# Kernel optimization log

Measured on AMD Instinct MI355X. Metric: run time of the kernel, lower is better.

## Reference

```python
import jax, jax.numpy as jnp
import numpy as np

D = 1024  # in_features == latent_dim
EPS = 1e-5


def _layernorm(x, g, b):
    mu = jnp.mean(x, axis=-1, keepdims=True)
    var = jnp.mean(jnp.square(x - mu), axis=-1, keepdims=True)
    return (x - mu) * jax.lax.rsqrt(var + EPS) * g + b


def setup_inputs() -> dict:
    key = jax.random.key(0)
    ks = jax.random.split(key, 8)
    s = 1.0 / np.sqrt(D)
    return {
        "x": jax.random.normal(ks[0], (4, 4096, D), dtype=jnp.float32),
        "w_qkv": jax.random.uniform(ks[1], (3 * D, D), jnp.float32, -s, s),
        "w_o": jax.random.uniform(ks[2], (D, D), jnp.float32, -s, s),
        "w1": jax.random.uniform(ks[3], (D, D), jnp.float32, -s, s),
        "b1": jax.random.uniform(ks[4], (D,), jnp.float32, -s, s),
        "w2": jax.random.uniform(ks[5], (D, D), jnp.float32, -s, s),
        "b2": jax.random.uniform(ks[6], (D,), jnp.float32, -s, s),
        "ln1_g": jnp.ones((D,), jnp.float32),
        "ln1_b": jnp.zeros((D,), jnp.float32),
        "ln2_g": jnp.ones((D,), jnp.float32),
        "ln2_b": jnp.zeros((D,), jnp.float32),
    }


def reference(x, w_qkv, w_o, w1, b1, w2, b2, ln1_g, ln1_b, ln2_g, ln2_b):
    B, S, _ = x.shape
    scale = 1.0 / np.sqrt(D * 1)  # 1/sqrt(latent_dim * n_heads), n_heads=1
    qkv = jnp.einsum("bsd,ed->bse", x, w_qkv)            # [B,S,3D]
    qkv = qkv.reshape(B, S, 1, 3 * D).transpose(0, 2, 1, 3)  # [B,1,S,3D]
    q, k, v = jnp.split(qkv, 3, axis=-1)                  # each [B,1,S,D]
    logits = jnp.einsum("bhid,bhjd->bhij", q, k) * scale  # [B,1,S,S]
    # Faithful quirk: softmax over the HEAD axis (dim=1). With 1 head this
    # yields an all-ones attention matrix.
    attn = jax.nn.softmax(logits, axis=1)
    vals = jnp.einsum("bhij,bhjd->bhid", attn, v)         # [B,1,S,D]
    vals = vals.transpose(0, 2, 1, 3).reshape(B, S, D)
    attn_out = jnp.einsum("bsd,ed->bse", vals, w_o)
    # squeeze(-2) is a no-op for S>1
    x = _layernorm(x + attn_out, ln1_g, ln1_b)
    h = jax.nn.gelu(jnp.einsum("bsd,ed->bse", x, w1) + b1, approximate=False)
    mlp_out = jnp.einsum("bsd,ed->bse", h, w2) + b2
    return _layernorm(x + mlp_out, ln2_g, ln2_b)
```

## Files before the change

kernel.cpp:

```cpp
#include <hip/hip_runtime.h>
#include <hip/hip_bf16.h>

typedef __hip_bfloat16 bf16;
typedef __attribute__((ext_vector_type(8))) short short8;
typedef __attribute__((ext_vector_type(4))) float f32x4;

#define DDIM 1024
#define SEQ  4096
#define NB   4
#define MTOT (NB*SEQ)

static __device__ __forceinline__ unsigned short f2bf(float f) {
    __hip_bfloat16 h = __float2bfloat16(f);
    unsigned short u; __builtin_memcpy(&u, &h, 2); return u;
}
static __device__ __forceinline__ float bf2f(unsigned short u) {
    __hip_bfloat16 h; __builtin_memcpy(&h, &u, 2); return __bfloat162float(h);
}

__global__ __launch_bounds__(256) void cast_w_kernel(
    const float* __restrict__ w1, const float* __restrict__ w2,
    unsigned short* __restrict__ w1b, unsigned short* __restrict__ w2b)
{
    size_t idx = ((size_t)blockIdx.x*256 + threadIdx.x) * 4;
    float4 a = *(const float4*)(w1 + idx);
    ushort4 o; o.x=f2bf(a.x); o.y=f2bf(a.y); o.z=f2bf(a.z); o.w=f2bf(a.w);
    *(ushort4*)(w1b + idx) = o;
    float4 b = *(const float4*)(w2 + idx);
    o.x=f2bf(b.x); o.y=f2bf(b.y); o.z=f2bf(b.z); o.w=f2bf(b.w);
    *(ushort4*)(w2b + idx) = o;
}

__global__ __launch_bounds__(256) void colsum_partial_kernel(
    const float* __restrict__ x, float* __restrict__ partial)
{
    int d  = blockIdx.x*256 + threadIdx.x;
    int b  = blockIdx.y;
    int sl = blockIdx.z;
    const float* p = x + ((size_t)b*SEQ + (size_t)sl*128)*DDIM + d;
    float s = 0.f;
    #pragma unroll 4
    for (int i = 0; i < 128; ++i) s += p[(size_t)i*DDIM];
    partial[((size_t)sl*NB + b)*DDIM + d] = s;
}

__global__ __launch_bounds__(256) void colsum_reduce_kernel(
    const float* __restrict__ partial, float* __restrict__ xsum)
{
    int d = blockIdx.x*256 + threadIdx.x;
    int b = blockIdx.y;
    float s = 0.f;
    #pragma unroll
    for (int sl = 0; sl < 32; ++sl) s += partial[((size_t)sl*NB + b)*DDIM + d];
    xsum[b*DDIM + d] = s;
}

__global__ __launch_bounds__(256) void matvec_kernel(
    const float* __restrict__ W, const float* __restrict__ vin, float* __restrict__ vout)
{
    int b = blockIdx.y;
    int g = threadIdx.x >> 4;
    int t = threadIdx.x & 15;
    int e = blockIdx.x*16 + g;
    const float* w = W + (size_t)e*DDIM;
    const float* v = vin + b*DDIM;
    float s = 0.f;
    for (int k = t; k < DDIM; k += 16) s += w[k]*v[k];
    #pragma unroll
    for (int o = 8; o; o >>= 1) s += __shfl_down(s, o, 16);
    if (t == 0) vout[b*DDIM + e] = s;
}

__global__ __launch_bounds__(256) void ln1_kernel(
    const float* __restrict__ x, const float* __restrict__ avec,
    const float* __restrict__ g1, const float* __restrict__ b1,
    unsigned short* __restrict__ x1b)
{
    int row = blockIdx.x;
    int b   = row >> 12;
    int tid = threadIdx.x;
    const float4* xr = (const float4*)(x + (size_t)row*DDIM);
    const float4* av = (const float4*)(avec + (size_t)b*DDIM);
    float4 xv = xr[tid], a4 = av[tid];
    float y0 = xv.x+a4.x, y1 = xv.y+a4.y, y2 = xv.z+a4.z, y3 = xv.w+a4.w;
    float s  = y0+y1+y2+y3;
    float ss = y0*y0+y1*y1+y2*y2+y3*y3;
    #pragma unroll
    for (int o = 32; o; o >>= 1) { s += __shfl_down(s,o,64); ss += __shfl_down(ss,o,64); }
    __shared__ float red[8];
    if ((tid&63) == 0) { red[tid>>6] = s; red[4+(tid>>6)] = ss; }
    __syncthreads();
    float St = red[0]+red[1]+red[2]+red[3];
    float Sq = red[4]+red[5]+red[6]+red[7];
    float mu = St*(1.0f/DDIM);
    float rs = rsqrtf(Sq*(1.0f/DDIM) - mu*mu + 1e-5f);
    float4 g4 = ((const float4*)g1)[tid];
    float4 bb = ((const float4*)b1)[tid];
    ushort4 o;
    o.x = f2bf((y0-mu)*rs*g4.x + bb.x);
    o.y = f2bf((y1-mu)*rs*g4.y + bb.y);
    o.z = f2bf((y2-mu)*rs*g4.z + bb.z);
    o.w = f2bf((y3-mu)*rs*g4.w + bb.w);
    *(ushort4*)(x1b + (size_t)row*DDIM + tid*4) = o;
}

__global__ __launch_bounds__(256, 3) void gemm_s32_kernel(
    const bf16* __restrict__ A, const bf16* __restrict__ Bw,
    const float* __restrict__ bias, unsigned short* __restrict__ outb)
{
    constexpr int K = 1024, N = 1024, BK = 32;
    __shared__ __align__(16) bf16 As[128*BK];
    __shared__ __align__(16) bf16 Bs[128*BK];
    const int tid  = threadIdx.x;
    const int wave = tid >> 6, lane = tid & 63;

    int bid = blockIdx.x;
    int swz = (bid & 7) * 128 + (bid >> 3);
    const size_t bm = (size_t)(swz >> 3) * 128;
    const size_t bn = (size_t)(swz & 7) * 128;

    const int wr = (wave >> 1) * 64, wc = (wave & 1) * 64;
    const int fr = lane & 15, fs = lane >> 4;

    const int srow = lane >> 2;
    const int sk   = (((lane & 3) ^ ((lane >> 3) & 3)) << 3);

    const int swo = (fs ^ ((fr >> 1) & 3)) << 4;

    f32x4 acc[4][4] = {};
    const bf16* Ab = A  + bm * K;
    const bf16* Bb = Bw + bn * K;

    for (int kt = 0; kt < K; kt += BK) {
        #pragma unroll
        for (int c = 0; c < 2; ++c) {
            int chunk = c*4 + wave;
            const bf16* ga = Ab + (size_t)(chunk*16 + srow)*K + kt + sk;
            const bf16* gb = Bb + (size_t)(chunk*16 + srow)*K + kt + sk;
            __builtin_amdgcn_global_load_lds(
                (const __attribute__((address_space(1))) void*)ga,
                (__attribute__((address_space(3))) void*)((char*)As + chunk*1024), 16, 0, 0);
            __builtin_amdgcn_global_load_lds(
                (const __attribute__((address_space(1))) void*)gb,
                (__attribute__((address_space(3))) void*)((char*)Bs + chunk*1024), 16, 0, 0);
        }
        __syncthreads();
        short8 af[4], bfr[4];
        #pragma unroll
        for (int m = 0; m < 4; ++m) af[m]  = *(const short8*)((char*)As + (wr + m*16 + fr)*64 + swo);
        #pragma unroll
        for (int n = 0; n < 4; ++n) bfr[n] = *(const short8*)((char*)Bs + (wc + n*16 + fr)*64 + swo);
        __builtin_amdgcn_s_setprio(1);
        #pragma unroll
        for (int m = 0; m < 4; ++m)
            #pragma unroll
            for (int n = 0; n < 4; ++n)
                acc[m][n] = __builtin_amdgcn_mfma_f32_16x16x32_bf16(af[m], bfr[n], acc[m][n], 0, 0, 0);
        __builtin_amdgcn_s_setprio(0);
        __syncthreads();
    }

    const int crow = fs * 4, ccol = fr;
    #pragma unroll
    for (int n = 0; n < 4; ++n) {
        size_t col = bn + wc + n*16 + ccol;
        float bv = bias[col];
        #pragma unroll
        for (int m = 0; m < 4; ++m) {
            #pragma unroll
            for (int r = 0; r < 4; ++r) {
                size_t row = bm + wr + m*16 + crow + r;
                float v = acc[m][n][r] + bv;
                float ge = 0.5f*v*(1.0f + erff(v*0.70710678118f));
                outb[row*(size_t)N + col] = f2bf(ge);
            }
        }
    }
}

__global__ __launch_bounds__(256, 2) void gemm2_kernel(
    const bf16* __restrict__ A, const bf16* __restrict__ Bw,
    const float* __restrict__ bias, unsigned short* __restrict__ xy,
    float2* __restrict__ part)
{
    constexpr int K = 1024, N = 1024, BK = 64, NT = K / BK;
    __shared__ __align__(16) bf16 lds[2][2][128*BK];
    const int tid  = threadIdx.x;
    const int wave = tid >> 6, lane = tid & 63;

    int bid = blockIdx.x;
    int swz = (bid & 7) * 128 + (bid >> 3);
    const size_t bm = (size_t)(swz >> 3) * 128;
    const size_t bn = (size_t)(swz & 7) * 128;

    const int wm = wave >> 1;
    const int wn = wave & 1;

    const int srow = tid >> 3;
    const int skel = (((tid & 7) ^ ((tid >> 3) & 7)) << 3);

    const int fr = lane & 15;
    const int fs = lane >> 4;
    int foff[2];
    #pragma unroll
    for (int ks = 0; ks < 2; ++ks)
        foff[ks] = fr*128 + (((ks*4 + fs) ^ (fr & 7)) << 4);

    f32x4 acc[4][4] = {};
    const bf16* Ab = A  + bm * K;
    const bf16* Bb = Bw + bn * K;

    auto stage = [&](int b, int kt) {
        #pragma unroll
        for (int mat = 0; mat < 2; ++mat) {
            const bf16* src = (mat == 0 ? Ab : Bb);
            #pragma unroll
            for (int g = 0; g < 4; ++g) {
                int row = g*32 + srow;
                const bf16* gp = src + (size_t)row * K + kt*BK + skel;
                __builtin_amdgcn_global_load_lds(
                    (const __attribute__((address_space(1))) void*)gp,
                    (__attribute__((address_space(3))) void*)
                        ((char*)&lds[b][mat][0] + g*4096 + wave*1024),
                    16, 0, 0);
            }
        }
    };

    stage(0, 0);

    #pragma unroll 2
    for (int t = 0; t < NT; ++t) {
        const int cur = t & 1;
        if (t < NT-1) {
            stage(cur ^ 1, t + 1);
            asm volatile("s_waitcnt vmcnt(8)" ::: "memory");
        } else {
            asm volatile("s_waitcnt vmcnt(0)" ::: "memory");
        }
        __builtin_amdgcn_s_barrier();

        const char* LA = (const char*)&lds[cur][0][0] + wm*8192;
        const char* LB = (const char*)&lds[cur][1][0] + wn*8192;
        #pragma unroll
        for (int ks = 0; ks < 2; ++ks) {
            short8 af[4], bfr[4];
            #pragma unroll
            for (int m = 0; m < 4; ++m) af[m]  = *(const short8*)(LA + m*2048 + foff[ks]);
            #pragma unroll
            for (int n = 0; n < 4; ++n) bfr[n] = *(const short8*)(LB + n*2048 + foff[ks]);
            __builtin_amdgcn_s_setprio(1);
            #pragma unroll
            for (int m = 0; m < 4; ++m)
                #pragma unroll
                for (int n = 0; n < 4; ++n)
                    acc[m][n] = __builtin_amdgcn_mfma_f32_16x16x32_bf16(
                        af[m], bfr[n], acc[m][n], 0, 0, 0);
            __builtin_amdgcn_s_setprio(0);
        }
        __builtin_amdgcn_s_barrier();
    }

    float vs[4][4] = {}, vq[4][4] = {};
    #pragma unroll
    for (int n = 0; n < 4; ++n) {
        size_t col = bn + wn*64 + n*16 + fr;
        float bv = bias[col];
        #pragma unroll
        for (int m = 0; m < 4; ++m) {
            #pragma unroll
            for (int r = 0; r < 4; ++r) {
                size_t row = bm + wm*64 + m*16 + fs*4 + r;
                size_t idx = row*(size_t)N + col;
                float v = acc[m][n][r] + bv + bf2f(xy[idx]);
                unsigned short qb = f2bf(v);
                xy[idx] = qb;
                float vv = bf2f(qb);
                vs[m][r] += vv;
                vq[m][r] += vv*vv;
            }
        }
    }
    #pragma unroll
    for (int o = 1; o < 16; o <<= 1) {
        #pragma unroll
        for (int m = 0; m < 4; ++m)
            #pragma unroll
            for (int r = 0; r < 4; ++r) {
                vs[m][r] += __shfl_xor(vs[m][r], o);
                vq[m][r] += __shfl_xor(vq[m][r], o);
            }
    }
    float* lred = (float*)&lds[0][0][0];
    if (fr == 0) {
        #pragma unroll
        for (int m = 0; m < 4; ++m)
            #pragma unroll
            for (int r = 0; r < 4; ++r) {
                int rl = wm*64 + m*16 + fs*4 + r;
                lred[(wn*128 + rl)*2]     = vs[m][r];
                lred[(wn*128 + rl)*2 + 1] = vq[m][r];
            }
    }
    __syncthreads();
    if (tid < 128) {
        float s  = lred[tid*2]       + lred[(128 + tid)*2];
        float sq = lred[tid*2 + 1]   + lred[(128 + tid)*2 + 1];
        part[(bm + tid)*8 + (bn >> 7)] = make_float2(s, sq);
    }
}

__global__ __launch_bounds__(256) void ln2_apply_kernel(
    const unsigned short* __restrict__ yb, const float2* __restrict__ part,
    const float* __restrict__ g2, const float* __restrict__ b2,
    float* __restrict__ out)
{
    int row = blockIdx.x;
    int tid = threadIdx.x;
    float s = 0.f, sq = 0.f;
    #pragma unroll
    for (int i = 0; i < 8; ++i) {
        float2 p = part[(size_t)row*8 + i];
        s += p.x; sq += p.y;
    }
    float mu = s * (1.0f/DDIM);
    float rs = rsqrtf(sq * (1.0f/DDIM) - mu*mu + 1e-5f);
    ushort4 yv = *(const ushort4*)(yb + (size_t)row*DDIM + tid*4);
    float4 g4 = ((const float4*)g2)[tid];
    float4 bb = ((const float4*)b2)[tid];
    float4 o;
    o.x = (bf2f(yv.x) - mu)*rs*g4.x + bb.x;
    o.y = (bf2f(yv.y) - mu)*rs*g4.y + bb.y;
    o.z = (bf2f(yv.z) - mu)*rs*g4.z + bb.z;
    o.w = (bf2f(yv.w) - mu)*rs*g4.w + bb.w;
    ((float4*)(out + (size_t)row*DDIM))[tid] = o;
}

extern "C" void kernel_launch(void* const* d_in, const int* in_sizes, int n_in,
                              void* d_out, int out_size, void* d_ws, size_t ws_size,
                              hipStream_t stream)
{
    const float* x     = (const float*)d_in[0];
    const float* w_qkv = (const float*)d_in[1];
    const float* w_o   = (const float*)d_in[2];
    const float* w1    = (const float*)d_in[3];
    const float* b1    = (const float*)d_in[4];
    const float* w2    = (const float*)d_in[5];
    const float* b2    = (const float*)d_in[6];
    const float* ln1g  = (const float*)d_in[7];
    const float* ln1b  = (const float*)d_in[8];
    const float* ln2g  = (const float*)d_in[9];
    const float* ln2b  = (const float*)d_in[10];
    float* out = (float*)d_out;
    char* ws = (char*)d_ws;

    unsigned short* x1b = (unsigned short*)(ws);
    unsigned short* hb  = (unsigned short*)(ws + 33554432);
    unsigned short* w1b = (unsigned short*)(ws + 67108864);
    unsigned short* w2b = (unsigned short*)(ws + 69206016);
    float* partial = (float*)(ws + 71303168);
    float* xsum    = (float*)(ws + 71827456);
    float* tvec    = (float*)(ws + 71843840);
    float* avec    = (float*)(ws + 71860224);
    float2* lnpart = (float2*)(ws + 67108864);

    cast_w_kernel<<<dim3(1024), 256, 0, stream>>>(w1, w2, w1b, w2b);
    colsum_partial_kernel<<<dim3(4, NB, 32), 256, 0, stream>>>(x, partial);
    colsum_reduce_kernel<<<dim3(4, NB), 256, 0, stream>>>(partial, xsum);
    matvec_kernel<<<dim3(64, NB), 256, 0, stream>>>(w_qkv + (size_t)2*DDIM*DDIM, xsum, tvec);
    matvec_kernel<<<dim3(64, NB), 256, 0, stream>>>(w_o, tvec, avec);
    ln1_kernel<<<dim3(MTOT), 256, 0, stream>>>(x, avec, ln1g, ln1b, x1b);
    gemm_s32_kernel<<<dim3(1024), 256, 0, stream>>>(
        (const bf16*)x1b, (const bf16*)w1b, b1, hb);
    gemm2_kernel<<<dim3(1024), 256, 0, stream>>>(
        (const bf16*)hb, (const bf16*)w2b, b2, x1b, lnpart);
    ln2_apply_kernel<<<dim3(MTOT), 256, 0, stream>>>(x1b, lnpart, ln2g, ln2b, out);
}
```

Baseline: 174.8 us.

## Double-buffer LDS tiles in first MLP GEMM with async prefetch

The first MLP GEMM now keeps two LDS buffers and issues the global-to-LDS loads for the next K tile before computing on the current one. It waits on vmcnt so only the previous tile's loads must finish, and uses raw s_barrier in place of __syncthreads. Launch bounds rise from 3 to 4 blocks per CU. The aim is to hide global load latency behind the MFMA work, at the cost of twice the LDS per block, which may limit occupancy.

```diff
diff --git a/kernel.cpp b/kernel.cpp
--- a/kernel.cpp
+++ b/kernel.cpp
@@ -104,13 +104,12 @@
     *(ushort4*)(x1b + (size_t)row*DDIM + tid*4) = o;
 }
 
-__global__ __launch_bounds__(256, 3) void gemm_s32_kernel(
+__global__ __launch_bounds__(256, 4) void gemm_bk32_kernel(
     const bf16* __restrict__ A, const bf16* __restrict__ Bw,
     const float* __restrict__ bias, unsigned short* __restrict__ outb)
 {
-    constexpr int K = 1024, N = 1024, BK = 32;
-    __shared__ __align__(16) bf16 As[128*BK];
-    __shared__ __align__(16) bf16 Bs[128*BK];
+    constexpr int K = 1024, N = 1024, BK = 32, NT = K / BK;
+    __shared__ __align__(16) bf16 lds[2][2][128*BK];
     const int tid  = threadIdx.x;
     const int wave = tid >> 6, lane = tid & 63;
 
@@ -122,8 +121,8 @@
     const int wr = (wave >> 1) * 64, wc = (wave & 1) * 64;
     const int fr = lane & 15, fs = lane >> 4;
 
-    const int srow = lane >> 2;
-    const int sk   = (((lane & 3) ^ ((lane >> 3) & 3)) << 3);
+    const int srow = tid >> 2;
+    const int sk   = (((tid & 3) ^ ((tid >> 3) & 3)) << 3);
 
     const int swo = (fs ^ ((fr >> 1) & 3)) << 4;
 
@@ -131,25 +130,42 @@
     const bf16* Ab = A  + bm * K;
     const bf16* Bb = Bw + bn * K;
 
-    for (int kt = 0; kt < K; kt += BK) {
-        #pragma unroll
-        for (int c = 0; c < 2; ++c) {
-            int chunk = c*4 + wave;
-            const bf16* ga = Ab + (size_t)(chunk*16 + srow)*K + kt + sk;
-            const bf16* gb = Bb + (size_t)(chunk*16 + srow)*K + kt + sk;
-            __builtin_amdgcn_global_load_lds(
-                (const __attribute__((address_space(1))) void*)ga,
-                (__attribute__((address_space(3))) void*)((char*)As + chunk*1024), 16, 0, 0);
-            __builtin_amdgcn_global_load_lds(
-                (const __attribute__((address_space(1))) void*)gb,
-                (__attribute__((address_space(3))) void*)((char*)Bs + chunk*1024), 16, 0, 0);
-        }
-        __syncthreads();
+    auto stage = [&](int b, int kt) {
+        #pragma unroll
+        for (int mat = 0; mat < 2; ++mat) {
+            const bf16* src = (mat == 0 ? Ab : Bb);
+            #pragma unroll
+            for (int g = 0; g < 2; ++g) {
+                const bf16* gp = src + (size_t)(g*64 + srow) * K + kt*BK + sk;
+                __builtin_amdgcn_global_load_lds(
+                    (const __attribute__((address_space(1))) void*)gp,
+                    (__attribute__((address_space(3))) void*)
+                        ((char*)&lds[b][mat][0] + g*4096 + wave*1024),
+                    16, 0, 0);
+            }
+        }
+    };
+
+    stage(0, 0);
+
+    #pragma unroll 2
+    for (int t = 0; t < NT; ++t) {
+        const int cur = t & 1;
+        if (t < NT-1) {
+            stage(cur ^ 1, t + 1);
+            asm volatile("s_waitcnt vmcnt(4)" ::: "memory");
+        } else {
+            asm volatile("s_waitcnt vmcnt(0)" ::: "memory");
+        }
+        __builtin_amdgcn_s_barrier();
+
+        const char* LA = (const char*)&lds[cur][0][0];
+        const char* LB = (const char*)&lds[cur][1][0];
         short8 af[4], bfr[4];
         #pragma unroll
-        for (int m = 0; m < 4; ++m) af[m]  = *(const short8*)((char*)As + (wr + m*16 + fr)*64 + swo);
-        #pragma unroll
-        for (int n = 0; n < 4; ++n) bfr[n] = *(const short8*)((char*)Bs + (wc + n*16 + fr)*64 + swo);
+        for (int m = 0; m < 4; ++m) af[m]  = *(const short8*)(LA + (wr + m*16 + fr)*64 + swo);
+        #pragma unroll
+        for (int n = 0; n < 4; ++n) bfr[n] = *(const short8*)(LB + (wc + n*16 + fr)*64 + swo);
         __builtin_amdgcn_s_setprio(1);
         #pragma unroll
         for (int m = 0; m < 4; ++m)
@@ -157,13 +173,13 @@
             for (int n = 0; n < 4; ++n)
                 acc[m][n] = __builtin_amdgcn_mfma_f32_16x16x32_bf16(af[m], bfr[n], acc[m][n], 0, 0, 0);
         __builtin_amdgcn_s_setprio(0);
-        __syncthreads();
-    }
-
-    const int crow = fs * 4, ccol = fr;
+        __builtin_amdgcn_s_barrier();
+    }
+
+    const int crow = fs * 4;
     #pragma unroll
     for (int n = 0; n < 4; ++n) {
-        size_t col = bn + wc + n*16 + ccol;
+        size_t col = bn + wc + n*16 + fr;
         float bv = bias[col];
         #pragma unroll
         for (int m = 0; m < 4; ++m) {
@@ -370,7 +386,7 @@
     matvec_kernel<<<dim3(64, NB), 256, 0, stream>>>(w_qkv + (size_t)2*DDIM*DDIM, xsum, tvec);
     matvec_kernel<<<dim3(64, NB), 256, 0, stream>>>(w_o, tvec, avec);
     ln1_kernel<<<dim3(MTOT), 256, 0, stream>>>(x, avec, ln1g, ln1b, x1b);
-    gemm_s32_kernel<<<dim3(1024), 256, 0, stream>>>(
+    gemm_bk32_kernel<<<dim3(1024), 256, 0, stream>>>(
         (const bf16*)x1b, (const bf16*)w1b, b1, hb);
     gemm2_kernel<<<dim3(1024), 256, 0, stream>>>(
         (const bf16*)hb, (const bf16*)w2b, b2, x1b, lnpart);
```

After: 173.0 us. Within noise of the previous version (-1.0%).

## Replace first MLP GEMM with 256x256-tile 8-wave double-buffered pipelined kernel

Applied to the files above, without the earlier changes.

Swaps the 128x128, BK=32, single-buffered GEMM1 (x1·w1ᵀ + bias + GELU) for a 256x256 tile kernel with 8 waves and 128 KB of dynamic LDS. Loads are double-buffered at BK=64 and interleaved with MFMA phases using explicit vmcnt/lgkmcnt waits and barriers. The aim is more data reuse per tile and overlap of global→LDS transfers with compute. In exchange it launches only 256 blocks at one block per CU, relies on fragile hand-placed waitcnts, and the larger accumulator file raises register pressure.

```diff
diff --git a/kernel.cpp b/kernel.cpp
--- a/kernel.cpp
+++ b/kernel.cpp
@@ -104,78 +104,120 @@
     *(ushort4*)(x1b + (size_t)row*DDIM + tid*4) = o;
 }
 
-__global__ __launch_bounds__(256, 3) void gemm_s32_kernel(
+__global__ __launch_bounds__(512, 1) void gemm8p_kernel(
     const bf16* __restrict__ A, const bf16* __restrict__ Bw,
     const float* __restrict__ bias, unsigned short* __restrict__ outb)
 {
-    constexpr int K = 1024, N = 1024, BK = 32;
-    __shared__ __align__(16) bf16 As[128*BK];
-    __shared__ __align__(16) bf16 Bs[128*BK];
+    extern __shared__ char smem[];
     const int tid  = threadIdx.x;
     const int wave = tid >> 6, lane = tid & 63;
 
     int bid = blockIdx.x;
-    int swz = (bid & 7) * 128 + (bid >> 3);
-    const size_t bm = (size_t)(swz >> 3) * 128;
-    const size_t bn = (size_t)(swz & 7) * 128;
-
-    const int wr = (wave >> 1) * 64, wc = (wave & 1) * 64;
+    int swz = (bid & 7) * 32 + (bid >> 3);
+    const size_t bm = (size_t)(swz >> 2) * 256;
+    const size_t bn = (size_t)(swz & 3) * 256;
+
+    const int wm = wave >> 2;
+    const int wn = wave & 3;
+
+    const int srow = tid >> 3;
+    const int skel = (((tid & 7) ^ ((tid >> 3) & 7)) << 3);
     const int fr = lane & 15, fs = lane >> 4;
 
-    const int srow = lane >> 2;
-    const int sk   = (((lane & 3) ^ ((lane >> 3) & 3)) << 3);
-
-    const int swo = (fs ^ ((fr >> 1) & 3)) << 4;
-
-    f32x4 acc[4][4] = {};
-    const bf16* Ab = A  + bm * K;
-    const bf16* Bb = Bw + bn * K;
-
-    for (int kt = 0; kt < K; kt += BK) {
-        #pragma unroll
-        for (int c = 0; c < 2; ++c) {
-            int chunk = c*4 + wave;
-            const bf16* ga = Ab + (size_t)(chunk*16 + srow)*K + kt + sk;
-            const bf16* gb = Bb + (size_t)(chunk*16 + srow)*K + kt + sk;
-            __builtin_amdgcn_global_load_lds(
-                (const __attribute__((address_space(1))) void*)ga,
-                (__attribute__((address_space(3))) void*)((char*)As + chunk*1024), 16, 0, 0);
-            __builtin_amdgcn_global_load_lds(
-                (const __attribute__((address_space(1))) void*)gb,
-                (__attribute__((address_space(3))) void*)((char*)Bs + chunk*1024), 16, 0, 0);
-        }
-        __syncthreads();
-        short8 af[4], bfr[4];
-        #pragma unroll
-        for (int m = 0; m < 4; ++m) af[m]  = *(const short8*)((char*)As + (wr + m*16 + fr)*64 + swo);
-        #pragma unroll
-        for (int n = 0; n < 4; ++n) bfr[n] = *(const short8*)((char*)Bs + (wc + n*16 + fr)*64 + swo);
-        __builtin_amdgcn_s_setprio(1);
-        #pragma unroll
-        for (int m = 0; m < 4; ++m)
-            #pragma unroll
-            for (int n = 0; n < 4; ++n)
-                acc[m][n] = __builtin_amdgcn_mfma_f32_16x16x32_bf16(af[m], bfr[n], acc[m][n], 0, 0, 0);
-        __builtin_amdgcn_s_setprio(0);
-        __syncthreads();
-    }
-
-    const int crow = fs * 4, ccol = fr;
-    #pragma unroll
-    for (int n = 0; n < 4; ++n) {
-        size_t col = bn + wc + n*16 + ccol;
+    const bf16* Ab = A  + bm * 1024;
+    const bf16* Bb = Bw + bn * 1024;
+
+#define REGN(d,mat,h) (smem + ((((d)<<2)|((mat)<<1)|(h))<<14))
+#define STAGE(dst, srcb, kt) { \
+    _Pragma("unroll") for (int g_ = 0; g_ < 2; ++g_) { \
+        const bf16* gp_ = (srcb) + (size_t)(g_*64 + srow)*1024 + (kt)*64 + skel; \
+        __builtin_amdgcn_global_load_lds( \
+            (const __attribute__((address_space(1))) void*)gp_, \
+            (__attribute__((address_space(3))) void*)((dst) + g_*8192 + wave*1024), \
+            16, 0, 0); } }
+#define RDA(d,kk,dst) { const char* ba_ = REGN(d,0,wm); \
+    _Pragma("unroll") for (int mf_ = 0; mf_ < 8; ++mf_) { \
+        int lr_ = mf_*16 + fr; int ph_ = ((kk)*4 + fs) ^ (lr_ & 7); \
+        dst[mf_] = *(const short8*)(ba_ + lr_*128 + ph_*16); } }
+#define RDB(d,kk,dst) { const char* bb_ = REGN(d,1,(wn>>1)); \
+    _Pragma("unroll") for (int nf_ = 0; nf_ < 4; ++nf_) { \
+        int lr_ = (wn&1)*64 + nf_*16 + fr; int ph_ = ((kk)*4 + fs) ^ (lr_ & 7); \
+        dst[nf_] = *(const short8*)(bb_ + lr_*128 + ph_*16); } }
+#define MM(AF,BF,NB_) { __builtin_amdgcn_s_setprio(1); \
+    _Pragma("unroll") for (int mf_ = 0; mf_ < 8; ++mf_) \
+        _Pragma("unroll") for (int nn_ = 0; nn_ < 2; ++nn_) \
+            acc[mf_][(NB_)+nn_] = __builtin_amdgcn_mfma_f32_16x16x32_bf16( \
+                AF[mf_], BF[(NB_)+nn_], acc[mf_][(NB_)+nn_], 0, 0, 0); \
+    __builtin_amdgcn_s_setprio(0); }
+#define BAR  __builtin_amdgcn_s_barrier()
+#define LGK0 asm volatile("s_waitcnt lgkmcnt(0)" ::: "memory")
+#define LGK8 asm volatile("s_waitcnt lgkmcnt(8)" ::: "memory")
+#define VM4  asm volatile("s_waitcnt vmcnt(4)"  ::: "memory")
+#define VM0  asm volatile("s_waitcnt vmcnt(0)"  ::: "memory")
+
+    short8 a0[8], a1[8], b0[4], b1[4];
+    f32x4 acc[8][4] = {};
+
+    STAGE(REGN(0,0,0), Ab,          0); STAGE(REGN(0,0,1), Ab + 128*1024, 0);
+    STAGE(REGN(0,1,0), Bb,          0); STAGE(REGN(0,1,1), Bb + 128*1024, 0);
+    STAGE(REGN(1,0,0), Ab,          1); STAGE(REGN(1,0,1), Ab + 128*1024, 1);
+    VM4;
+    BAR;
+
+    for (int j = 0; j < 8; ++j) {
+        const int k1 = 2*j + 1, k2 = 2*j + 2, k3 = 2*j + 3;
+        const bool t2 = (k2 < 16), t3 = (k3 < 16);
+        RDA(0,0,a0); RDB(0,0,b0);
+        STAGE(REGN(1,1,0), Bb, k1);
+        LGK8;
+        BAR; LGK0; MM(a0,b0,0); BAR;
+        RDA(0,1,a1);
+        STAGE(REGN(1,1,1), Bb + 128*1024, k1);
+        BAR; LGK0; MM(a0,b0,2); BAR;
+        RDB(0,1,b1);
+        if (t2) STAGE(REGN(0,0,0), Ab, k2);
+        BAR; LGK0; MM(a1,b1,0); BAR;
+        if (t2) { STAGE(REGN(0,0,1), Ab + 128*1024, k2); VM4; } else { VM0; }
+        BAR; LGK0; MM(a1,b1,2); BAR;
+        RDA(1,0,a0); RDB(1,0,b0);
+        if (t2) STAGE(REGN(0,1,0), Bb, k2);
+        LGK8;
+        BAR; LGK0; MM(a0,b0,0); BAR;
+        RDA(1,1,a1);
+        if (t2) STAGE(REGN(0,1,1), Bb + 128*1024, k2);
+        BAR; LGK0; MM(a0,b0,2); BAR;
+        RDB(1,1,b1);
+        if (t3) STAGE(REGN(1,0,0), Ab, k3);
+        BAR; LGK0; MM(a1,b1,0); BAR;
+        if (t3) { STAGE(REGN(1,0,1), Ab + 128*1024, k3); VM4; }
+        BAR; LGK0; MM(a1,b1,2); BAR;
+    }
+
+    #pragma unroll
+    for (int nf = 0; nf < 4; ++nf) {
+        size_t col = bn + wn*64 + nf*16 + fr;
         float bv = bias[col];
         #pragma unroll
-        for (int m = 0; m < 4; ++m) {
-            #pragma unroll
-            for (int r = 0; r < 4; ++r) {
-                size_t row = bm + wr + m*16 + crow + r;
-                float v = acc[m][n][r] + bv;
+        for (int mf = 0; mf < 8; ++mf) {
+            #pragma unroll
+            for (int rr = 0; rr < 4; ++rr) {
+                size_t row = bm + wm*128 + mf*16 + fs*4 + rr;
+                float v = acc[mf][nf][rr] + bv;
                 float ge = 0.5f*v*(1.0f + erff(v*0.70710678118f));
-                outb[row*(size_t)N + col] = f2bf(ge);
+                outb[row*1024 + col] = f2bf(ge);
             }
         }
     }
+#undef REGN
+#undef STAGE
+#undef RDA
+#undef RDB
+#undef MM
+#undef BAR
+#undef LGK0
+#undef LGK8
+#undef VM4
+#undef VM0
 }
 
 __global__ __launch_bounds__(256, 2) void gemm2_kernel(
@@ -364,13 +406,16 @@
     float* avec    = (float*)(ws + 71860224);
     float2* lnpart = (float2*)(ws + 67108864);
 
+    (void)hipFuncSetAttribute((const void*)gemm8p_kernel,
+                              hipFuncAttributeMaxDynamicSharedMemorySize, 131072);
+
     cast_w_kernel<<<dim3(1024), 256, 0, stream>>>(w1, w2, w1b, w2b);
     colsum_partial_kernel<<<dim3(4, NB, 32), 256, 0, stream>>>(x, partial);
     colsum_reduce_kernel<<<dim3(4, NB), 256, 0, stream>>>(partial, xsum);
     matvec_kernel<<<dim3(64, NB), 256, 0, stream>>>(w_qkv + (size_t)2*DDIM*DDIM, xsum, tvec);
     matvec_kernel<<<dim3(64, NB), 256, 0, stream>>>(w_o, tvec, avec);
     ln1_kernel<<<dim3(MTOT), 256, 0, stream>>>(x, avec, ln1g, ln1b, x1b);
-    gemm_s32_kernel<<<dim3(1024), 256, 0, stream>>>(
+    gemm8p_kernel<<<dim3(256), 512, 131072, stream>>>(
         (const bf16*)x1b, (const bf16*)w1b, b1, hb);
     gemm2_kernel<<<dim3(1024), 256, 0, stream>>>(
         (const bf16*)hb, (const bf16*)w2b, b2, x1b, lnpart);
```

After: 171.6 us. Within noise of the previous version (-1.8%).
